# Kernel tuning notes

Hardware: AMD Instinct MI355X
Metric: run time of the kernel (lower is better)

The kernel has to match this reference:

```python
import jax, jax.numpy as jnp
import numpy as np

# Dimensions: B=batch, T=timesteps, D=input_dim, U=units, R=recurrent_size, NE=#edge types
B, T, D, U, R, NE = 1024, 128, 256, 256, 4, 40


def setup_inputs() -> dict:
    key = jax.random.key(0)
    ks = jax.random.split(key, 11)
    s = 1.0 / np.sqrt(U)  # RandomUniform(-1/sqrt(units), 1/sqrt(units)) as in __init__
    inputs = jax.random.normal(ks[0], (B, T, D), jnp.float32)
    input_lengths = jax.random.randint(ks[1], (B,), 1, T + 1)
    # dependencies[b, t, k] indexes a PAST timestep (< t) whose hidden state feeds step t;
    # values >= t are treated as '$' (no dependency -> zero state), matching the string-'$' logic.
    dependencies = jax.random.randint(ks[2], (B, T, R - 1), 0, T)
    edge_types = jax.random.randint(ks[3], (B, T, R), 0, NE)
    mask = jax.random.randint(ks[4], (B, T), 0, 2).astype(bool)
    cell_mask = jax.random.randint(ks[5], (B, T, R), 0, 2).astype(bool)
    Wx = jax.random.uniform(ks[6], (D, 3 * U), jnp.float32, -s, s)   # input kernel (r,z,h)
    Uh = jax.random.uniform(ks[7], (U, 3 * U), jnp.float32, -s, s)   # recurrent kernel (r,z,h)
    Ve = jax.random.uniform(ks[8], (U, 3 * U), jnp.float32, -s, s)   # edge-embedding kernel (r,z,h)
    b = jax.random.uniform(ks[9], (3 * U,), jnp.float32, -s, s)
    edge_emb = jax.random.normal(ks[10], (NE, U), jnp.float32) * 0.02  # shared_emb table
    return dict(inputs=inputs, input_lengths=input_lengths, dependencies=dependencies,
                edge_types=edge_types, mask=mask, cell_mask=cell_mask,
                Wx=Wx, Uh=Uh, Ve=Ve, b=b, edge_emb=edge_emb)


def _graph_gru_forward(inputs, dependencies, edge_types, mask, cell_mask, Wx, Uh, Ve, b, edge_emb):
    Bn, Tn, Dn = inputs.shape
    Un = Uh.shape[0]
    # time-major, as the wrapper does with swap_batch_timestep
    xg_t = jnp.einsum('btd,dg->tbg', inputs, Wx) + b   # precompute input projections [T,B,3U]
    dep_t = jnp.swapaxes(dependencies, 0, 1)           # [T,B,R-1]
    et_t = jnp.swapaxes(edge_types, 0, 1)              # [T,B,R]
    m_t = jnp.swapaxes(mask, 0, 1)                     # [T,B]
    cm_t = jnp.swapaxes(cell_mask, 0, 1)               # [T,B,R]
    bidx = jnp.arange(Bn)

    def step(carry, xs):
        h_prev, H = carry                  # h_prev: [B,U]; H: running history of states [T,B,U]
        t, xg, dep, et, m, cm = xs
        # gather dependency states from history; dep >= t means '$' -> zero state
        valid = dep < t                                        # [B,R-1]
        dep_states = H[jnp.clip(dep, 0, Tn - 1), bidx[:, None]]  # [B,R-1,U]
        dep_states = jnp.where(valid[..., None], dep_states, 0.0)
        hs = jnp.concatenate([h_prev[:, None, :], dep_states], axis=1)  # states tuple -> [B,R,U]
        cmf = cm.astype(hs.dtype)[..., None]                   # per-slot cell mask [B,R,1]
        hs_m = hs * cmf
        e_m = edge_emb[et] * cmf                               # [B,R,U]
        # aggregate messages from the R masked (state, edge-embedding) slots into the 3 gates
        msg = jnp.einsum('bru,ug->bg', hs_m, Uh) + jnp.einsum('bru,ug->bg', e_m, Ve)  # [B,3U]
        xr, xz, xh = jnp.split(xg, 3, axis=-1)
        mr, mz, mh = jnp.split(msg, 3, axis=-1)
        r = jax.nn.sigmoid(xr + mr)
        z = jax.nn.sigmoid(xz + mz)
        hcand = jnp.tanh(xh + r * mh)
        denom = jnp.maximum(cmf.sum(axis=1), 1.0)              # [B,1]
        h_bar = hs_m.sum(axis=1) / denom                       # mean of active predecessor states
        h_new = z * h_bar + (1.0 - z) * hcand
        # masked update: where(mask_t, new_state, previous return state)
        h_out = jnp.where(m[:, None], h_new, h_prev)
        H = H.at[t].set(h_out)
        return (h_out, H), None

    h0 = jnp.zeros((Bn, Un), inputs.dtype)
    H0 = jnp.zeros((Tn, Bn, Un), inputs.dtype)
    (h_last, _), _ = jax.lax.scan(
        step, (h0, H0), (jnp.arange(Tn), xg_t, dep_t, et_t, m_t, cm_t))
    # zero_output_for_mask on the last output (return_sequences=False)
    return jnp.where(m_t[-1][:, None], h_last, 0.0)


def reference(inputs, input_lengths, dependencies, edge_types, mask, cell_mask,
              Wx, Uh, Ve, b, edge_emb):
    # input_lengths only matters when go_backwards=True (default False) -> unused.
    del input_lengths
    return _graph_gru_forward(inputs, dependencies, edge_types, mask, cell_mask,
                              Wx, Uh, Ve, b, edge_emb)
```

## Files before the change

### kernel.cpp

```cpp
#include <hip/hip_runtime.h>
#include <hip/hip_bf16.h>
#include <stdint.h>

typedef _Float16 f16;
typedef _Float16 f16x8 __attribute__((ext_vector_type(8)));
typedef _Float16 f16x4 __attribute__((ext_vector_type(4)));
typedef float    f32x4 __attribute__((ext_vector_type(4)));

#define B_N 1024
#define T_N 128
#define U_N 256
#define G3  768
#define NC  1024
#define KC  512
#define M_N (B_N * T_N)
#define S16P 264

__device__ __forceinline__ void glds16(const void* g, void* l) {
  __builtin_amdgcn_global_load_lds((const __attribute__((address_space(1))) unsigned int*)g,
                                   (__attribute__((address_space(3))) unsigned int*)l, 16, 0, 0);
}
__device__ __forceinline__ void glds4(const void* g, void* l) {
  __builtin_amdgcn_global_load_lds((const __attribute__((address_space(1))) unsigned int*)g,
                                   (__attribute__((address_space(3))) unsigned int*)l, 4, 0, 0);
}

__global__ void k_prep(const float* __restrict__ Wx, const float* __restrict__ Uh,
                       const float* __restrict__ Ve, const float* __restrict__ bsrc,
                       f16* __restrict__ WcatT, float* __restrict__ bias, f16* __restrict__ UhF)
{
  int idx = blockIdx.x * 256 + threadIdx.x;
  if (idx < NC * KC) {
    int np = idx >> 9, k = idx & 511;
    int u = np >> 2, part = np & 3;
    float v;
    if (part == 0)      v = (k < 256) ? Wx[k * G3 + u]         : Ve[(k - 256) * G3 + u];
    else if (part == 1) v = (k < 256) ? Wx[k * G3 + 256 + u]   : Ve[(k - 256) * G3 + 256 + u];
    else if (part == 2) v = (k < 256) ? Wx[k * G3 + 512 + u]   : 0.f;
    else                v = (k < 256) ? 0.f                    : Ve[(k - 256) * G3 + 512 + u];
    WcatT[np * KC + k] = (f16)v;
    return;
  }
  int i2 = idx - NC * KC;
  if (i2 < U_N * G3) {
    int j = i2 & 7, lane = (i2 >> 3) & 63, fn = i2 >> 9;
    int nt = fn % 6, kkw = fn / 6;
    int kk = kkw & 7, w = kkw >> 3;
    int k = kk * 32 + (lane >> 4) * 8 + j;
    int npp = w * 96 + nt * 16 + (lane & 15);
    int q = npp >> 4;
    int u = (q / 3) * 16 + (npp & 15), gate = q % 3;
    UhF[i2] = (f16)Uh[k * G3 + gate * 256 + u];
    return;
  }
  int i3 = i2 - U_N * G3;
  if (i3 < NC) {
    int u = i3 >> 2, part = i3 & 3;
    bias[i3] = (part < 3) ? bsrc[part * 256 + u] : 0.f;
  }
}

__global__ __launch_bounds__(256) void k_build_a(const float* __restrict__ inp, const int* __restrict__ et,
                          const int* __restrict__ cmk, const float* __restrict__ emb,
                          f16* __restrict__ A)
{
  int m  = blockIdx.x * 4 + (threadIdx.x >> 6);
  int u4 = (threadIdx.x & 63) * 4;
  const int* e = et  + (size_t)m * 4;
  const int* c = cmk + (size_t)m * 4;
  f32x4 em = {0.f, 0.f, 0.f, 0.f};
  #pragma unroll
  for (int r = 0; r < 4; ++r)
    if (c[r]) em += *(const f32x4*)(emb + e[r] * U_N + u4);
  f32x4 x = *(const f32x4*)(inp + (size_t)m * 256 + u4);
  f16x4 xa, ea;
  #pragma unroll
  for (int j = 0; j < 4; ++j) { xa[j] = (f16)x[j]; ea[j] = (f16)em[j]; }
  *(f16x4*)(A + (size_t)m * KC + u4)       = xa;
  *(f16x4*)(A + (size_t)m * KC + 256 + u4) = ea;
}

__global__ __launch_bounds__(256) void k_gemm(const f16* __restrict__ A,
                                              const f16* __restrict__ BT,
                                              const float* __restrict__ bias,
                                              f16* __restrict__ C)
{
  __shared__ f16 sA[128 * 32];
  __shared__ f16 sB[128 * 32];
  const int tid  = threadIdx.x;
  const int lane = tid & 63, wv = tid >> 6;
  const int wm = wv >> 1, wn = wv & 1;
  const int wg = (blockIdx.x & 7) * 1024 + (blockIdx.x >> 3);
  const int m0 = (wg >> 3) * 128;
  const int n0 = (wg & 7)  * 128;

  f32x4 acc[4][4] = {};

  for (int kt = 0; kt < 16; ++kt) {
    const int k0 = kt * 32;
    #pragma unroll
    for (int is = 0; is < 2; ++is) {
      int t2  = is * 256 + tid;
      int row = t2 >> 2, c = t2 & 3;
      f16x8 va = *(const f16x8*)(A  + (size_t)(m0 + row) * KC + k0 + c * 8);
      *(f16x8*)(sA + row * 32 + ((c ^ (row & 3)) * 8)) = va;
      f16x8 vb = *(const f16x8*)(BT + (size_t)(n0 + row) * KC + k0 + c * 8);
      *(f16x8*)(sB + row * 32 + ((c ^ (row & 3)) * 8)) = vb;
    }
    __syncthreads();

    const int kb = lane >> 4;
    f16x8 af[4], bf[4];
    #pragma unroll
    for (int i = 0; i < 4; ++i) {
      int ar = wm * 64 + i * 16 + (lane & 15);
      af[i] = *(const f16x8*)(sA + ar * 32 + ((kb ^ (ar & 3)) * 8));
      int br = wn * 64 + i * 16 + (lane & 15);
      bf[i] = *(const f16x8*)(sB + br * 32 + ((kb ^ (br & 3)) * 8));
    }
    #pragma unroll
    for (int i = 0; i < 4; ++i)
      #pragma unroll
      for (int j = 0; j < 4; ++j)
        acc[i][j] = __builtin_amdgcn_mfma_f32_16x16x32_f16(af[i], bf[j], acc[i][j], 0, 0, 0);
    __syncthreads();
  }

  #pragma unroll
  for (int i = 0; i < 4; ++i)
    #pragma unroll
    for (int j = 0; j < 4; ++j) {
      int col = n0 + wn * 64 + j * 16 + (lane & 15);
      float bv = bias[col];
      #pragma unroll
      for (int r = 0; r < 4; ++r) {
        int row = m0 + wm * 64 + i * 16 + (lane >> 4) * 4 + r;
        C[(size_t)row * NC + col] = (f16)(acc[i][j][r] + bv);
      }
    }
}

__global__ __launch_bounds__(512, 2) void k_scan4(
    const f16* __restrict__ pre,
    const f16* __restrict__ UhF,
    const int* __restrict__ dep,
    const int* __restrict__ cmk,
    const int* __restrict__ msk,
    f16* __restrict__ H16,
    float* __restrict__ out)
{
  __shared__ __align__(16) f16 s16[16 * S16P];
  __shared__ __align__(16) f16 hring[2][1024];
  __shared__ __align__(16) f16 dbuf[2][3072];
  __shared__ __align__(16) f16 spre[3][4096];
  __shared__ __align__(16) int sidxl[4][64];
  __shared__ __align__(16) int dpad[64];

  const int tid  = threadIdx.x;
  const int lane = tid & 63, w = tid >> 6;
  const int l15  = lane & 15, lhi = lane >> 4;
  const int b0   = blockIdx.x * 4;

  f16x8 uh[48];
  {
    const f16* ub = UhF + ((size_t)w * 48 * 64 + lane) * 8;
    #pragma unroll
    for (int i = 0; i < 48; ++i) uh[i] = *(const f16x8*)(ub + i * 512);
  }

  ((int*)hring)[tid]       = 0;
  ((int*)hring)[tid + 512] = 0;

  if (tid < 96) {
    int tt = tid >> 5, ll2 = tid & 31, rr = ll2 >> 3, f = ll2 & 7;
    size_t b = b0 + rr;
    int v;
    if (f < 4)      v = cmk[(b * T_N + tt) * 4 + f];
    else if (f < 7) v = dep[(b * T_N + tt) * 3 + (f - 4)];
    else            v = msk[b * T_N + tt];
    sidxl[tt][rr * 8 + f] = v;
  }
  __syncthreads();

  const f16* spre_src = pre + ((size_t)(b0 + (w >> 1)) * T_N) * 1024 + (w & 1) * 512 + lane * 8;
  const int  ll = lane & 31;
  const int  srr = ll >> 3, sf = ll & 7;
  const size_t sb = b0 + srr;
  const int* sidx_base;
  int sidx_stride;
  if (sf < 4)      { sidx_base = cmk + sb * T_N * 4 + sf;       sidx_stride = 4; }
  else if (sf < 7) { sidx_base = dep + sb * T_N * 3 + (sf - 4); sidx_stride = 3; }
  else             { sidx_base = msk + sb * T_N;                sidx_stride = 1; }
  const int dq  = 2 * w + (lane >> 5);
  const int drr = dq / 3, drm = dq - drr * 3;
  const f16* dsrc_base = H16 + (size_t)(b0 + drr) * 256 + (lane & 31) * 8;
  const int strr = ((w - 6) * 64 + lane) >> 5;
  const int stuo = (((w - 6) * 64 + lane) & 31) * 8;

  #pragma unroll
  for (int pr = 0; pr < 2; ++pr)
    glds16(spre_src + (size_t)pr * 1024, &spre[pr][w * 512]);
  #pragma unroll
  for (int i = 0; i < 3; ++i)
    glds4(msk, &dpad[0]);

  for (int t = 0; t < T_N; ++t) {
    asm volatile("s_waitcnt vmcnt(2)" ::: "memory");
    __builtin_amdgcn_sched_barrier(0);

    if (tid < 128) {
      const int rr = tid >> 5, uo = (tid & 31) * 8;
      const int* six = &sidxl[t & 3][rr * 8];
      int cm0 = six[0];
      int cms0 = six[1], cms1 = six[2], cms2 = six[3];
      int dd0 = six[4],  dd1 = six[5],  dd2 = six[6];
      f16x8 hprev = *(const f16x8*)&hring[(t + 1) & 1][rr * 256 + uo];
      f16x8 hold  = *(const f16x8*)&hring[t & 1][rr * 256 + uo];
      f32x4 a0 = {0.f,0.f,0.f,0.f}, a1 = {0.f,0.f,0.f,0.f};
      if (cm0) {
        #pragma unroll
        for (int j = 0; j < 4; ++j) { a0[j] += (float)hprev[j]; a1[j] += (float)hprev[j + 4]; }
      }
      int cma[3] = {cms0, cms1, cms2};
      int dda[3] = {dd0, dd1, dd2};
      #pragma unroll
      for (int r = 0; r < 3; ++r) {
        f16x8 dv = *(const f16x8*)&dbuf[t & 1][(rr * 3 + r) * 256 + uo];
        int d = dda[r];
        f16x8 src = (d == t - 1) ? hprev : ((d == t - 2) ? hold : dv);
        if (cma[r] && (d < t)) {
          #pragma unroll
          for (int j = 0; j < 4; ++j) { a0[j] += (float)src[j]; a1[j] += (float)src[j + 4]; }
        }
      }
      f16x8 s8;
      #pragma unroll
      for (int j = 0; j < 4; ++j) { s8[j] = (f16)a0[j]; s8[j + 4] = (f16)a1[j]; }
      *(f16x8*)&s16[(rr * 4) * S16P + uo] = s8;
    }
    asm volatile("s_waitcnt lgkmcnt(0)" ::: "memory");
    __builtin_amdgcn_s_barrier();
    __builtin_amdgcn_sched_barrier(0);

    if (w < 6) {
      int d = sidxl[(t + 1) & 3][drr * 8 + 4 + drm];
      glds16(dsrc_base + (size_t)d * (B_N * 256), &dbuf[(t + 1) & 1][w * 512]);
    } else {
      f16x8 hv = *(const f16x8*)&hring[(t + 1) & 1][strr * 256 + stuo];
      int tt = (t == 0) ? T_N : (t - 1);
      *(f16x8*)(H16 + ((size_t)tt * B_N + b0 + strr) * 256 + stuo) = hv;
    }
    __builtin_amdgcn_sched_barrier(0);
    {
      int tt2 = (t + 2 < T_N) ? (t + 2) : (T_N - 1);
      glds16(spre_src + (size_t)tt2 * 1024, &spre[(t + 2) % 3][w * 512]);
    }
    __builtin_amdgcn_sched_barrier(0);
    {
      int t3 = (t + 3 < T_N) ? (t + 3) : (T_N - 1);
      glds4(sidx_base + (size_t)t3 * sidx_stride, &sidxl[(t + 3) & 3][0]);
    }
    __builtin_amdgcn_sched_barrier(0);

    f32x4 acc[6];
    #pragma unroll
    for (int i = 0; i < 6; ++i) acc[i] = (f32x4){0.f, 0.f, 0.f, 0.f};
    #pragma unroll
    for (int kk = 0; kk < 8; ++kk) {
      f16x8 a = *(const f16x8*)(s16 + l15 * S16P + kk * 32 + lhi * 8);
      #pragma unroll
      for (int nt = 0; nt < 6; ++nt)
        acc[nt] = __builtin_amdgcn_mfma_f32_16x16x32_f16(a, uh[kk * 6 + nt], acc[nt], 0, 0, 0);
    }

    asm volatile("s_waitcnt vmcnt(7)" ::: "memory");
    __builtin_amdgcn_sched_barrier(0);
    {
      const int* six = &sidxl[t & 3][lhi * 8];
      int c0 = six[0], c1 = six[1], c2 = six[2], c3 = six[3];
      int mfl = six[7];
      float cnt  = (float)(c0 + c1 + c2 + c3);
      float rcnt = __builtin_amdgcn_rcpf(fmaxf(cnt, 1.f));
      #pragma unroll
      for (int ub2 = 0; ub2 < 2; ++ub2) {
        int u = w * 32 + ub2 * 16 + l15;
        f16x4 p = *(const f16x4*)&spre[t % 3][lhi * 1024 + u * 4];
        float mr = acc[ub2 * 3 + 0][0];
        float mz = acc[ub2 * 3 + 1][0];
        float mh = acc[ub2 * 3 + 2][0];
        float tr = (float)p.x + mr;
        float tz = (float)p.y + mz;
        float hx = (float)p.z;
        float he = (float)p.w;
        float rg = __builtin_amdgcn_rcpf(1.f + __expf(-tr));
        float zg = __builtin_amdgcn_rcpf(1.f + __expf(-tz));
        float aa = hx + rg * (mh + he);
        float hc = 2.f * __builtin_amdgcn_rcpf(1.f + __expf(-2.f * aa)) - 1.f;
        float sv = (float)s16[(lhi * 4) * S16P + u];
        float hb = sv * rcnt;
        float hn = zg * hb + (1.f - zg) * hc;
        float hp_ = (float)hring[(t + 1) & 1][lhi * 256 + u];
        float ho = mfl ? hn : hp_;
        hring[t & 1][lhi * 256 + u] = (f16)ho;
      }
    }
    asm volatile("s_waitcnt lgkmcnt(0)" ::: "memory");
    __builtin_amdgcn_s_barrier();
    __builtin_amdgcn_sched_barrier(0);
  }

  if (tid < 128) {
    const int rr = tid >> 5, uo = (tid & 31) * 8;
    int m = sidxl[(T_N - 1) & 3][rr * 8 + 7];
    f16x8 h8 = *(const f16x8*)&hring[(T_N - 1) & 1][rr * 256 + uo];
    f32x4 o0, o1;
    #pragma unroll
    for (int j = 0; j < 4; ++j) {
      o0[j] = m ? (float)h8[j]     : 0.f;
      o1[j] = m ? (float)h8[j + 4] : 0.f;
    }
    *(f32x4*)(out + (size_t)(b0 + rr) * 256 + uo)     = o0;
    *(f32x4*)(out + (size_t)(b0 + rr) * 256 + uo + 4) = o1;
  }
}

extern "C" void kernel_launch(void* const* d_in, const int* in_sizes, int n_in,
                              void* d_out, int out_size, void* d_ws, size_t ws_size,
                              hipStream_t stream)
{
  const float* inputs = (const float*)d_in[0];
  const int*   deps   = (const int*)d_in[2];
  const int*   et     = (const int*)d_in[3];
  const int*   msk    = (const int*)d_in[4];
  const int*   cmk    = (const int*)d_in[5];
  const float* Wx     = (const float*)d_in[6];
  const float* Uh     = (const float*)d_in[7];
  const float* Ve     = (const float*)d_in[8];
  const float* bb     = (const float*)d_in[9];
  const float* emb    = (const float*)d_in[10];
  float* out = (float*)d_out;

  char* ws = (char*)d_ws;
  f16*   A     = (f16*)ws;
  f16*   H16   = (f16*)ws;
  f16*   pre   = (f16*)(ws + 134217728);
  f16*   WcatT = (f16*)(ws + 402653184);
  float* bias  = (float*)(ws + 403701760);
  f16*   UhF   = (f16*)(ws + 403705856);

  int prep_n = NC * KC + U_N * G3 + NC;
  k_prep<<<dim3((prep_n + 255) / 256), dim3(256), 0, stream>>>(Wx, Uh, Ve, bb, WcatT, bias, UhF);
  k_build_a<<<dim3(M_N / 4), dim3(256), 0, stream>>>(inputs, et, cmk, emb, A);
  k_gemm<<<dim3((M_N / 128) * (NC / 128)), dim3(256), 0, stream>>>(A, WcatT, bias, pre);
  k_scan4<<<dim3(B_N / 4), dim3(512), 0, stream>>>(pre, UhF, deps, cmk, msk, H16, out);
}
```

Baseline: 579.6 us.

## Pre-tile GEMM operands and pipeline loads via direct global-to-LDS triple buffering

```diff
diff --git a/kernel.cpp b/kernel.cpp
--- a/kernel.cpp
+++ b/kernel.cpp
@@ -27,18 +27,22 @@
 
 __global__ void k_prep(const float* __restrict__ Wx, const float* __restrict__ Uh,
                        const float* __restrict__ Ve, const float* __restrict__ bsrc,
-                       f16* __restrict__ WcatT, float* __restrict__ bias, f16* __restrict__ UhF)
+                       f16* __restrict__ B2, float* __restrict__ bias, f16* __restrict__ UhF)
 {
   int idx = blockIdx.x * 256 + threadIdx.x;
   if (idx < NC * KC) {
-    int np = idx >> 9, k = idx & 511;
+    int e = idx & 7, slot = (idx >> 3) & 3, r = (idx >> 5) & 127;
+    int kt = (idx >> 12) & 15, nt8 = idx >> 16;
+    int swz = ((r >> 2) ^ r) & 3;
+    int np = nt8 * 128 + r;
+    int k  = kt * 32 + ((slot ^ swz) & 3) * 8 + e;
     int u = np >> 2, part = np & 3;
     float v;
     if (part == 0)      v = (k < 256) ? Wx[k * G3 + u]         : Ve[(k - 256) * G3 + u];
     else if (part == 1) v = (k < 256) ? Wx[k * G3 + 256 + u]   : Ve[(k - 256) * G3 + 256 + u];
     else if (part == 2) v = (k < 256) ? Wx[k * G3 + 512 + u]   : 0.f;
     else                v = (k < 256) ? 0.f                    : Ve[(k - 256) * G3 + 512 + u];
-    WcatT[np * KC + k] = (f16)v;
+    B2[idx] = (f16)v;
     return;
   }
   int i2 = idx - NC * KC;
@@ -60,84 +64,132 @@
   }
 }
 
-__global__ __launch_bounds__(256) void k_build_a(const float* __restrict__ inp, const int* __restrict__ et,
-                          const int* __restrict__ cmk, const float* __restrict__ emb,
-                          f16* __restrict__ A)
+__global__ __launch_bounds__(256) void k_build_a2(const float* __restrict__ inp, const int* __restrict__ et,
+                           const int* __restrict__ cmk, const float* __restrict__ emb,
+                           f16* __restrict__ A2)
 {
-  int m  = blockIdx.x * 4 + (threadIdx.x >> 6);
-  int u4 = (threadIdx.x & 63) * 4;
-  const int* e = et  + (size_t)m * 4;
-  const int* c = cmk + (size_t)m * 4;
-  f32x4 em = {0.f, 0.f, 0.f, 0.f};
-  #pragma unroll
-  for (int r = 0; r < 4; ++r)
-    if (c[r]) em += *(const f32x4*)(emb + e[r] * U_N + u4);
-  f32x4 x = *(const f32x4*)(inp + (size_t)m * 256 + u4);
-  f16x4 xa, ea;
-  #pragma unroll
-  for (int j = 0; j < 4; ++j) { xa[j] = (f16)x[j]; ea[j] = (f16)em[j]; }
-  *(f16x4*)(A + (size_t)m * KC + u4)       = xa;
-  *(f16x4*)(A + (size_t)m * KC + 256 + u4) = ea;
-}
-
-__global__ __launch_bounds__(256) void k_gemm(const f16* __restrict__ A,
-                                              const f16* __restrict__ BT,
-                                              const float* __restrict__ bias,
-                                              f16* __restrict__ C)
+  int idx = blockIdx.x * 256 + threadIdx.x;
+  int slot = idx & 3, t = (idx >> 2) & 127, kt = (idx >> 9) & 15, b = idx >> 13;
+  int swz = ((t >> 2) ^ t) & 3;
+  int k0 = kt * 32 + ((slot ^ swz) & 3) * 8;
+  int m = b * 128 + t;
+  f16x8 v;
+  if (k0 < 256) {
+    const float* s = inp + (size_t)m * 256 + k0;
+    #pragma unroll
+    for (int j = 0; j < 8; ++j) v[j] = (f16)s[j];
+  } else {
+    int c = k0 - 256;
+    const int* e  = et  + (size_t)m * 4;
+    const int* cm = cmk + (size_t)m * 4;
+    float a[8] = {0,0,0,0,0,0,0,0};
+    #pragma unroll
+    for (int r = 0; r < 4; ++r)
+      if (cm[r]) {
+        const float* es = emb + e[r] * U_N + c;
+        #pragma unroll
+        for (int j = 0; j < 8; ++j) a[j] += es[j];
+      }
+    #pragma unroll
+    for (int j = 0; j < 8; ++j) v[j] = (f16)a[j];
+  }
+  *(f16x8*)(A2 + (size_t)idx * 8) = v;
+}
+
+__global__ __launch_bounds__(256) void k_gemm2(const f16* __restrict__ A2,
+                                               const f16* __restrict__ B2,
+                                               const float* __restrict__ bias,
+                                               f16* __restrict__ C)
 {
-  __shared__ f16 sA[128 * 32];
-  __shared__ f16 sB[128 * 32];
+  __shared__ __align__(16) f16 sbuf[3][2][4096];
   const int tid  = threadIdx.x;
   const int lane = tid & 63, wv = tid >> 6;
   const int wm = wv >> 1, wn = wv & 1;
+  const int l15 = lane & 15, lhi = lane >> 4;
   const int wg = (blockIdx.x & 7) * 1024 + (blockIdx.x >> 3);
-  const int m0 = (wg >> 3) * 128;
-  const int n0 = (wg & 7)  * 128;
+  const int mt = wg >> 3, nt = wg & 7;
+  const int m0 = mt * 128, n0 = nt * 128;
+
+  const f16* gabase = A2 + (size_t)mt * 16 * 4096 + wv * 1024 + lane * 8;
+  const f16* gbbase = B2 + (size_t)nt * 16 * 4096 + wv * 1024 + lane * 8;
+
+  #define STAGE(kt_, buf_) do {                                             \
+    int kk_ = (kt_);                                                        \
+    glds16(gabase + (size_t)kk_ * 4096,       &sbuf[buf_][0][wv * 1024]);   \
+    glds16(gabase + (size_t)kk_ * 4096 + 512, &sbuf[buf_][0][wv * 1024 + 512]); \
+    glds16(gbbase + (size_t)kk_ * 4096,       &sbuf[buf_][1][wv * 1024]);   \
+    glds16(gbbase + (size_t)kk_ * 4096 + 512, &sbuf[buf_][1][wv * 1024 + 512]); \
+  } while (0)
 
   f32x4 acc[4][4] = {};
 
-  for (int kt = 0; kt < 16; ++kt) {
-    const int k0 = kt * 32;
-    #pragma unroll
-    for (int is = 0; is < 2; ++is) {
-      int t2  = is * 256 + tid;
-      int row = t2 >> 2, c = t2 & 3;
-      f16x8 va = *(const f16x8*)(A  + (size_t)(m0 + row) * KC + k0 + c * 8);
-      *(f16x8*)(sA + row * 32 + ((c ^ (row & 3)) * 8)) = va;
-      f16x8 vb = *(const f16x8*)(BT + (size_t)(n0 + row) * KC + k0 + c * 8);
-      *(f16x8*)(sB + row * 32 + ((c ^ (row & 3)) * 8)) = vb;
-    }
-    __syncthreads();
-
-    const int kb = lane >> 4;
+  STAGE(0, 0);
+  STAGE(1, 1);
+  __builtin_amdgcn_sched_barrier(0);
+
+  int aoff[4], boff[4];
+  #pragma unroll
+  for (int i = 0; i < 4; ++i) {
+    int ar = wm * 64 + i * 16 + l15;
+    aoff[i] = ar * 32 + ((lhi ^ ((ar >> 2) ^ ar)) & 3) * 8;
+    int br = wn * 64 + i * 16 + l15;
+    boff[i] = br * 32 + ((lhi ^ ((br >> 2) ^ br)) & 3) * 8;
+  }
+
+  for (int t = 0; t < 16; ++t) {
+    const int buf  = t % 3;
+    const int bufp = (t + 2) % 3;
+    STAGE((t + 2 < 16) ? (t + 2) : 15, bufp);
+    __builtin_amdgcn_sched_barrier(0);
+    asm volatile("s_waitcnt vmcnt(8)" ::: "memory");
+    __builtin_amdgcn_sched_barrier(0);
+    __builtin_amdgcn_s_barrier();
+    __builtin_amdgcn_sched_barrier(0);
+
+    const f16* sA = &sbuf[buf][0][0];
+    const f16* sB = &sbuf[buf][1][0];
     f16x8 af[4], bf[4];
     #pragma unroll
     for (int i = 0; i < 4; ++i) {
-      int ar = wm * 64 + i * 16 + (lane & 15);
-      af[i] = *(const f16x8*)(sA + ar * 32 + ((kb ^ (ar & 3)) * 8));
-      int br = wn * 64 + i * 16 + (lane & 15);
-      bf[i] = *(const f16x8*)(sB + br * 32 + ((kb ^ (br & 3)) * 8));
+      af[i] = *(const f16x8*)(sA + aoff[i]);
+      bf[i] = *(const f16x8*)(sB + boff[i]);
     }
     #pragma unroll
     for (int i = 0; i < 4; ++i)
       #pragma unroll
       for (int j = 0; j < 4; ++j)
         acc[i][j] = __builtin_amdgcn_mfma_f32_16x16x32_f16(af[i], bf[j], acc[i][j], 0, 0, 0);
-    __syncthreads();
-  }
-
+
+    asm volatile("s_waitcnt lgkmcnt(0)" ::: "memory");
+    __builtin_amdgcn_s_barrier();
+    __builtin_amdgcn_sched_barrier(0);
+  }
+
+  float bv[4];
+  #pragma unroll
+  for (int j = 0; j < 4; ++j) bv[j] = bias[n0 + wn * 64 + j * 16 + l15];
+  asm volatile("s_waitcnt vmcnt(0)" ::: "memory");
+  __builtin_amdgcn_sched_barrier(0);
+  __builtin_amdgcn_s_barrier();
+
+  f16* ep = &sbuf[0][0][0];
   #pragma unroll
   for (int i = 0; i < 4; ++i)
     #pragma unroll
-    for (int j = 0; j < 4; ++j) {
-      int col = n0 + wn * 64 + j * 16 + (lane & 15);
-      float bv = bias[col];
-      #pragma unroll
-      for (int r = 0; r < 4; ++r) {
-        int row = m0 + wm * 64 + i * 16 + (lane >> 4) * 4 + r;
-        C[(size_t)row * NC + col] = (f16)(acc[i][j][r] + bv);
-      }
-    }
+    for (int j = 0; j < 4; ++j)
+      #pragma unroll
+      for (int r = 0; r < 4; ++r)
+        ep[(wm * 64 + i * 16 + lhi * 4 + r) * 132 + wn * 64 + j * 16 + l15] =
+            (f16)(acc[i][j][r] + bv[j]);
+  __syncthreads();
+
+  #pragma unroll
+  for (int it = 0; it < 8; ++it) {
+    int row = it * 16 + (tid >> 4), chunk = tid & 15;
+    *(f16x8*)(C + (size_t)(m0 + row) * 1024 + n0 + chunk * 8) =
+        *(const f16x8*)(ep + row * 132 + chunk * 8);
+  }
+  #undef STAGE
 }
 
 __global__ __launch_bounds__(512, 2) void k_scan4(
@@ -341,16 +393,16 @@
   float* out = (float*)d_out;
 
   char* ws = (char*)d_ws;
-  f16*   A     = (f16*)ws;
+  f16*   A2    = (f16*)ws;
   f16*   H16   = (f16*)ws;
   f16*   pre   = (f16*)(ws + 134217728);
-  f16*   WcatT = (f16*)(ws + 402653184);
+  f16*   B2    = (f16*)(ws + 402653184);
   float* bias  = (float*)(ws + 403701760);
   f16*   UhF   = (f16*)(ws + 403705856);
 
   int prep_n = NC * KC + U_N * G3 + NC;
-  k_prep<<<dim3((prep_n + 255) / 256), dim3(256), 0, stream>>>(Wx, Uh, Ve, bb, WcatT, bias, UhF);
-  k_build_a<<<dim3(M_N / 4), dim3(256), 0, stream>>>(inputs, et, cmk, emb, A);
-  k_gemm<<<dim3((M_N / 128) * (NC / 128)), dim3(256), 0, stream>>>(A, WcatT, bias, pre);
+  k_prep<<<dim3((prep_n + 255) / 256), dim3(256), 0, stream>>>(Wx, Uh, Ve, bb, B2, bias, UhF);
+  k_build_a2<<<dim3(M_N * 64 / 256), dim3(256), 0, stream>>>(inputs, et, cmk, emb, A2);
+  k_gemm2<<<dim3((M_N / 128) * (NC / 128)), dim3(256), 0, stream>>>(A2, B2, bias, pre);
   k_scan4<<<dim3(B_N / 4), dim3(512), 0, stream>>>(pre, UhF, deps, cmk, msk, H16, out);
 }
```

Result: faster. 507.3 us (-12.5%).
